# Performance work log

Hardware: AMD Instinct MI355X
Metric: run time of the kernel (lower is better)

## Reference

```python
import jax, jax.numpy as jnp
import numpy as np


def setup_inputs() -> dict:
    key = jax.random.key(0)
    ks = jax.random.split(key, 7)
    B, N, D, A = 16, 2048, 256, 256
    s = 1.0 / np.sqrt(D)
    return {
        "x": jax.random.normal(ks[0], (B, N, D), dtype=jnp.float32),
        "W1": jax.random.normal(ks[1], (D, A), dtype=jnp.float32) * s,
        "b1": jnp.zeros((A,), dtype=jnp.float32),
        "W2": jax.random.normal(ks[2], (D, A), dtype=jnp.float32) * s,
        "b2": jnp.zeros((A,), dtype=jnp.float32),
        "W3": jax.random.normal(ks[3], (D, A), dtype=jnp.float32) * s,
        "b3": jnp.zeros((A,), dtype=jnp.float32),
    }


def reference(x, W1, b1, W2, b2, W3, b3):
    # x: [B, N, D]
    Q = x @ W1 + b1  # [B, N, A]
    K = x @ W2 + b2  # [B, N, A]
    V = x @ W3 + b3  # [B, N, A]
    # unscaled attention scores, as in the original (no 1/sqrt(d))
    scores = jnp.einsum("bqa,bka->bqk", Q, K)  # [B, N, N]
    weights = jax.nn.softmax(scores, axis=-1)
    ctx = jnp.einsum("bqk,bka->bqa", weights, V)  # [B, N, A]
    return ctx.sum(axis=1)  # [B, A] (squeeze is a no-op for B>1)
```

## Files before the change

### kernel.cpp

```cpp
#include <hip/hip_runtime.h>
#include <hip/hip_bf16.h>
#include <stdint.h>

typedef unsigned short u16;
typedef __attribute__((ext_vector_type(8)))  short    s16x8;
typedef __attribute__((ext_vector_type(8)))  _Float16 f16x8;
typedef __attribute__((ext_vector_type(16))) float    f32x16;

#define B_DIM 16
#define N_SEQ 2048
#define M_TOT (B_DIM * N_SEQ)
#define LOG2E 1.44269504088896f
#define SHIFT 64.0f

static __device__ __forceinline__ f32x16 MFMA16(f16x8 a, f16x8 b, f32x16 c) {
  return __builtin_amdgcn_mfma_f32_32x32x16_f16(a, b, c, 0, 0, 0);
}

static __device__ __forceinline__ void stage_f16(
    const u16* __restrict__ src, char* ldsbuf, int row0, int t)
{
#pragma unroll
  for (int jj = 0; jj < 4; ++jj) {
    const int row = (t >> 5) + jj * 8;
    const int sl  = (t & 31) ^ (t >> 5);
    const char* g = (const char*)src + ((size_t)(row0 + row) * 512 + (size_t)sl * 16);
    __builtin_amdgcn_global_load_lds(
        (const __attribute__((address_space(1))) uint32_t*)g,
        (__attribute__((address_space(3))) uint32_t*)(ldsbuf + t * 16 + jj * 4096),
        16, 0, 0);
  }
}

#define SWZ8(bid, G_, J_)                                      \
  const int xcd_ = (bid) & 7, r_ = (bid) >> 3;                 \
  const int J_ = r_ & 7;                                       \
  const int G_ = ((r_ >> 3) << 3) | xcd_;

__global__ void splitW_kernel(const float* __restrict__ W1, const float* __restrict__ W2,
                              u16* __restrict__ WTf) {
  const int gid = blockIdx.x * 256 + threadIdx.x;
  const int a = gid >> 8, k = gid & 255;
  const float v = (a < 256) ? W1[k * 256 + a] * LOG2E : W2[k * 256 + (a - 256)];
  WTf[gid] = __builtin_bit_cast(u16, (_Float16)v);
}

__global__ __launch_bounds__(256, 2) void proj_kernel(
    const float* __restrict__ x, const u16* __restrict__ WTf,
    const float* __restrict__ b1, const float* __restrict__ b2,
    u16* __restrict__ Qf, u16* __restrict__ Kf)
{
  __shared__ char lds[32768];
  const int t = threadIdx.x, wv = t >> 6, ln = t & 63, lr = ln & 31, g = ln >> 5;
  const int ablk = blockIdx.x & 3;
  const int m0 = (blockIdx.x >> 2) * 256;
  const int aglob = ablk * 128 + wv * 32 + lr;

  f16x8 wf[16];
  {
    const u16* base = WTf + (size_t)aglob * 256 + g * 8;
#pragma unroll
    for (int c = 0; c < 16; ++c) wf[c] = *(const f16x8*)(base + c * 16);
  }
  const float bias = (aglob < 256) ? b1[aglob] * LOG2E : b2[aglob - 256];
  u16* Of = (ablk < 2) ? Qf : Kf;
  const int acol = aglob & 255;

  const int srow = t >> 3;
  const int scol = (t & 7) * 32;

  float4 v[8];
  {
    const float* src = x + (size_t)(m0 + srow) * 256 + scol;
#pragma unroll
    for (int j = 0; j < 8; ++j) v[j] = *(const float4*)(src + j * 4);
#pragma unroll
    for (int q8 = 0; q8 < 4; ++q8) {
      float ff[8] = {v[q8*2].x, v[q8*2].y, v[q8*2].z, v[q8*2].w,
                     v[q8*2+1].x, v[q8*2+1].y, v[q8*2+1].z, v[q8*2+1].w};
      f16x8 H;
#pragma unroll
      for (int e = 0; e < 8; ++e) H[e] = (_Float16)ff[e];
      const int swz = (((t & 7) * 4 + q8) ^ (srow & 7));
      *(f16x8*)(lds + srow * 512 + swz * 16) = H;
    }
  }
  __syncthreads();
  int p = 0;
  for (int it = 0; it < 8; ++it) {
    if (it + 1 < 8) {
      const float* src = x + (size_t)(m0 + (it + 1) * 32 + srow) * 256 + scol;
#pragma unroll
      for (int j = 0; j < 8; ++j) v[j] = *(const float4*)(src + j * 4);
    }
    const char* bh = lds + p * 16384;
    f32x16 S = {};
#pragma unroll
    for (int cc = 0; cc < 16; ++cc) {
      const int sl = ((cc * 2 + g) ^ (lr & 7)) * 16;
      const f16x8 a = *(const f16x8*)(bh + lr * 512 + sl);
      S = MFMA16(a, wf[cc], S);
    }
#pragma unroll
    for (int i = 0; i < 16; ++i) {
      const int mrow = m0 + it * 32 + (i & 3) + 8 * (i >> 2) + 4 * g;
      const float val = S[i] + bias;
      Of[(size_t)mrow * 256 + acol] = __builtin_bit_cast(u16, (_Float16)val);
    }
    if (it + 1 < 8) {
      char* bp = lds + (p ^ 1) * 16384;
#pragma unroll
      for (int q8 = 0; q8 < 4; ++q8) {
        float ff[8] = {v[q8*2].x, v[q8*2].y, v[q8*2].z, v[q8*2].w,
                       v[q8*2+1].x, v[q8*2+1].y, v[q8*2+1].z, v[q8*2+1].w};
        f16x8 H;
#pragma unroll
        for (int e = 0; e < 8; ++e) H[e] = (_Float16)ff[e];
        const int swz = (((t & 7) * 4 + q8) ^ (srow & 7));
        *(f16x8*)(bp + srow * 512 + swz * 16) = H;
      }
    }
    __syncthreads();
    p ^= 1;
  }
}

__global__ __launch_bounds__(256, 2) void pass1_kernel(
    const u16* __restrict__ Qf, const u16* __restrict__ Kf,
    float* __restrict__ lsum)
{
  __shared__ char lds[32768];
  SWZ8(blockIdx.x, grp, qg);
  const int b = grp >> 2, kq = grp & 3;
  const int t = threadIdx.x, wv = t >> 6, ln = t & 63, lr = ln & 31, gg = ln >> 5;

  const int q0 = b * 2048 + qg * 256 + wv * 64;
  f16x8 qf0[16], qf1[16];
  {
    const u16* qb0 = Qf + (size_t)(q0 + lr) * 256 + gg * 8;
    const u16* qb1 = qb0 + 32 * 256;
#pragma unroll
    for (int c = 0; c < 16; ++c) {
      qf0[c] = *(const f16x8*)(qb0 + c * 16);
      qf1[c] = *(const f16x8*)(qb1 + c * 16);
    }
  }
  const int k0 = b * 2048 + kq * 512;

  stage_f16(Kf, lds, k0, t);
  __syncthreads();
  float l0 = 0.f, l1 = 0.f;
  int pp = 0;
  for (int it = 0; it < 16; ++it) {
    if (it + 1 < 16) stage_f16(Kf, lds + (pp ^ 1) * 16384, k0 + (it + 1) * 32, t);
    const char* bh = lds + pp * 16384;
    f32x16 S0, S1;
#pragma unroll
    for (int i = 0; i < 16; ++i) { S0[i] = -SHIFT; S1[i] = -SHIFT; }
#pragma unroll
    for (int c = 0; c < 16; ++c) {
      const int sl = ((c * 2 + gg) ^ (lr & 7)) * 16;
      const f16x8 a = *(const f16x8*)(bh + lr * 512 + sl);
      S0 = MFMA16(a, qf0[c], S0);
      S1 = MFMA16(a, qf1[c], S1);
    }
    float r0 = 0.f, r1 = 0.f;
#pragma unroll
    for (int i = 0; i < 16; ++i) { r0 += exp2f(S0[i]); r1 += exp2f(S1[i]); }
    l0 += r0; l1 += r1;
    __syncthreads();
    pp ^= 1;
  }
  l0 += __shfl_xor(l0, 32);
  l1 += __shfl_xor(l1, 32);
  if (ln < 32) {
    atomicAdd(&lsum[q0 + ln],      l0);
    atomicAdd(&lsum[q0 + 32 + ln], l1);
  }
}

__global__ __launch_bounds__(256, 2) void pass2_kernel(
    const u16* __restrict__ Qf, const u16* __restrict__ Kf,
    const float* __restrict__ lsum, float* __restrict__ cvec)
{
  __shared__ char lds[32768];
  SWZ8(blockIdx.x, grp, kg);
  const int b = grp >> 2, qq = grp & 3;
  const int t = threadIdx.x, wv = t >> 6, ln = t & 63, lr = ln & 31, gg = ln >> 5;

  const int k0 = b * 2048 + kg * 256 + wv * 64;
  f16x8 kf0[16], kf1[16];
  {
    const u16* kb0 = Kf + (size_t)(k0 + lr) * 256 + gg * 8;
    const u16* kb1 = kb0 + 32 * 256;
#pragma unroll
    for (int c = 0; c < 16; ++c) {
      kf0[c] = *(const f16x8*)(kb0 + c * 16);
      kf1[c] = *(const f16x8*)(kb1 + c * 16);
    }
  }
  const int q0 = b * 2048 + qq * 512;

  float ck0[16], ck1[16];
#pragma unroll
  for (int i = 0; i < 16; ++i) { ck0[i] = 0.f; ck1[i] = 0.f; }

  stage_f16(Qf, lds, q0, t);
  __syncthreads();
  int pp = 0;
  for (int it = 0; it < 16; ++it) {
    if (it + 1 < 16) stage_f16(Qf, lds + (pp ^ 1) * 16384, q0 + (it + 1) * 32, t);
    const float il = 1.0f / fmaxf(lsum[q0 + it * 32 + lr], 1e-30f);
    const char* bh = lds + pp * 16384;
    f32x16 S0, S1;
#pragma unroll
    for (int i = 0; i < 16; ++i) { S0[i] = -SHIFT; S1[i] = -SHIFT; }
#pragma unroll
    for (int c = 0; c < 16; ++c) {
      const int sl = ((c * 2 + gg) ^ (lr & 7)) * 16;
      const f16x8 qa = *(const f16x8*)(bh + lr * 512 + sl);
      S0 = MFMA16(kf0[c], qa, S0);
      S1 = MFMA16(kf1[c], qa, S1);
    }
#pragma unroll
    for (int i = 0; i < 16; ++i) {
      ck0[i] += exp2f(S0[i]) * il;
      ck1[i] += exp2f(S1[i]) * il;
    }
    __syncthreads();
    pp ^= 1;
  }
#pragma unroll
  for (int i = 0; i < 16; ++i) {
#pragma unroll
    for (int d = 1; d <= 16; d <<= 1) {
      ck0[i] += __shfl_xor(ck0[i], d);
      ck1[i] += __shfl_xor(ck1[i], d);
    }
  }
  if (lr == 0) {
#pragma unroll
    for (int i = 0; i < 16; ++i) {
      const int klocal = (i & 3) + 8 * (i >> 2) + 4 * gg;
      atomicAdd(&cvec[k0 + klocal],      ck0[i]);
      atomicAdd(&cvec[k0 + 32 + klocal], ck1[i]);
    }
  }
}

__global__ void reducey_kernel(const float* __restrict__ x, const float* __restrict__ cvec,
                               float* __restrict__ yv, float* __restrict__ sumc) {
  const int b = blockIdx.x >> 4, kc = blockIdx.x & 15, tid = threadIdx.x;
  const float* xb = x + ((size_t)b * 2048 + kc * 128) * 256;
  const float* cb = cvec + b * 2048 + kc * 128;
  float a0 = 0.f, a1 = 0.f, a2 = 0.f, a3 = 0.f;
  for (int k = 0; k < 128; k += 4) {
    a0 = fmaf(cb[k],     xb[(size_t)k * 256 + tid],       a0);
    a1 = fmaf(cb[k + 1], xb[(size_t)(k + 1) * 256 + tid], a1);
    a2 = fmaf(cb[k + 2], xb[(size_t)(k + 2) * 256 + tid], a2);
    a3 = fmaf(cb[k + 3], xb[(size_t)(k + 3) * 256 + tid], a3);
  }
  atomicAdd(&yv[b * 256 + tid], (a0 + a1) + (a2 + a3));
  if (tid == 0) {
    float s = 0.f;
    for (int k = 0; k < 128; ++k) s += cb[k];
    atomicAdd(&sumc[b], s);
  }
}

__global__ void final_kernel(const float* __restrict__ yv, const float* __restrict__ sumc,
                             const float* __restrict__ W3, const float* __restrict__ b3,
                             float* __restrict__ out) {
  __shared__ float ys[256];
  const int b = blockIdx.x, a = threadIdx.x;
  ys[a] = yv[b * 256 + a];
  __syncthreads();
  float acc = sumc[b] * b3[a];
#pragma unroll 4
  for (int d = 0; d < 256; ++d) acc = fmaf(ys[d], W3[d * 256 + a], acc);
  out[b * 256 + a] = acc;
}

extern "C" void kernel_launch(void* const* d_in, const int* in_sizes, int n_in,
                              void* d_out, int out_size, void* d_ws, size_t ws_size,
                              hipStream_t stream) {
  const float* x  = (const float*)d_in[0];
  const float* W1 = (const float*)d_in[1];
  const float* b1 = (const float*)d_in[2];
  const float* W2 = (const float*)d_in[3];
  const float* b2 = (const float*)d_in[4];
  const float* W3 = (const float*)d_in[5];
  const float* b3 = (const float*)d_in[6];
  float* out = (float*)d_out;

  char* ws = (char*)d_ws;
  const size_t SZ_WT = 512u * 256u * 2u;
  const size_t SZ_QK = (size_t)M_TOT * 256u * 2u;
  u16* WTf = (u16*)(ws);                 ws += SZ_WT;
  u16* Qf  = (u16*)(ws);                 ws += SZ_QK;
  u16* Kf  = (u16*)(ws);                 ws += SZ_QK;
  float* lsum = (float*)(ws);            ws += (size_t)M_TOT * 4u;
  float* cvec = (float*)(ws);            ws += (size_t)M_TOT * 4u;
  float* yv   = (float*)(ws);            ws += 4096u * 4u;
  float* sumc = (float*)(ws);            ws += 64u;

  hipMemsetAsync(lsum, 0, (size_t)M_TOT * 8u + 4096u * 4u + 64u, stream);

  splitW_kernel<<<dim3(512), dim3(256), 0, stream>>>(W1, W2, WTf);
  proj_kernel<<<dim3(512), dim3(256), 0, stream>>>(x, WTf, b1, b2, Qf, Kf);
  pass1_kernel<<<dim3(512), dim3(256), 0, stream>>>(Qf, Kf, lsum);
  pass2_kernel<<<dim3(512), dim3(256), 0, stream>>>(Qf, Kf, lsum, cvec);
  reducey_kernel<<<dim3(256), dim3(256), 0, stream>>>(x, cvec, yv, sumc);
  final_kernel<<<dim3(16), dim3(256), 0, stream>>>(yv, sumc, W3, b3, out);
}
```

Before: 229.5 us.

## Stage 64-row K/Q tiles, precompute inverse sums, use hardware exp2 and setprio

pass1 and pass2 now stage 64-row tiles per iteration in a 64KB double-buffered dynamic LDS region, halving the number of barriers and iterations. pass2 precomputes the reciprocal softmax sums into LDS up front instead of doing a global load and division every iteration. Both passes use the hardware exp2 builtin and raise wave priority around the MFMA loops. proj_kernel switches to 512-thread blocks that each cover one of Q or K, which halves the number of blocks and the x loads per thread. The larger LDS footprint may reduce how many blocks fit on a CU.

```diff
diff --git a/kernel.cpp b/kernel.cpp
--- a/kernel.cpp
+++ b/kernel.cpp
@@ -3,7 +3,6 @@
 #include <stdint.h>
 
 typedef unsigned short u16;
-typedef __attribute__((ext_vector_type(8)))  short    s16x8;
 typedef __attribute__((ext_vector_type(8)))  _Float16 f16x8;
 typedef __attribute__((ext_vector_type(16))) float    f32x16;
 
@@ -13,18 +12,24 @@
 #define LOG2E 1.44269504088896f
 #define SHIFT 64.0f
 
+#if __has_builtin(__builtin_amdgcn_exp2f)
+#define EXP2(x) __builtin_amdgcn_exp2f(x)
+#else
+#define EXP2(x) exp2f(x)
+#endif
+
 static __device__ __forceinline__ f32x16 MFMA16(f16x8 a, f16x8 b, f32x16 c) {
   return __builtin_amdgcn_mfma_f32_32x32x16_f16(a, b, c, 0, 0, 0);
 }
 
-static __device__ __forceinline__ void stage_f16(
+static __device__ __forceinline__ void stage64(
     const u16* __restrict__ src, char* ldsbuf, int row0, int t)
 {
 #pragma unroll
-  for (int jj = 0; jj < 4; ++jj) {
-    const int row = (t >> 5) + jj * 8;
-    const int sl  = (t & 31) ^ (t >> 5);
-    const char* g = (const char*)src + ((size_t)(row0 + row) * 512 + (size_t)sl * 16);
+  for (int jj = 0; jj < 8; ++jj) {
+    const int sl = (t & 31) ^ (t >> 5);
+    const char* g = (const char*)src +
+        ((size_t)(row0 + (t >> 5) + jj * 8) * 512 + (size_t)sl * 16);
     __builtin_amdgcn_global_load_lds(
         (const __attribute__((address_space(1))) uint32_t*)g,
         (__attribute__((address_space(3))) uint32_t*)(ldsbuf + t * 16 + jj * 4096),
@@ -45,43 +50,42 @@
   WTf[gid] = __builtin_bit_cast(u16, (_Float16)v);
 }
 
-__global__ __launch_bounds__(256, 2) void proj_kernel(
+__global__ __launch_bounds__(512, 2) void proj_kernel(
     const float* __restrict__ x, const u16* __restrict__ WTf,
     const float* __restrict__ b1, const float* __restrict__ b2,
     u16* __restrict__ Qf, u16* __restrict__ Kf)
 {
   __shared__ char lds[32768];
   const int t = threadIdx.x, wv = t >> 6, ln = t & 63, lr = ln & 31, g = ln >> 5;
-  const int ablk = blockIdx.x & 3;
-  const int m0 = (blockIdx.x >> 2) * 256;
-  const int aglob = ablk * 128 + wv * 32 + lr;
+  const int ablk = blockIdx.x & 1;
+  const int m0 = (blockIdx.x >> 1) * 256;
+  const int aglob = wv * 32 + lr;
 
   f16x8 wf[16];
   {
-    const u16* base = WTf + (size_t)aglob * 256 + g * 8;
+    const u16* base = WTf + ((size_t)ablk * 256 + aglob) * 256 + g * 8;
 #pragma unroll
     for (int c = 0; c < 16; ++c) wf[c] = *(const f16x8*)(base + c * 16);
   }
-  const float bias = (aglob < 256) ? b1[aglob] * LOG2E : b2[aglob - 256];
-  u16* Of = (ablk < 2) ? Qf : Kf;
-  const int acol = aglob & 255;
-
-  const int srow = t >> 3;
-  const int scol = (t & 7) * 32;
-
-  float4 v[8];
+  const float bias = (ablk == 0) ? b1[aglob] * LOG2E : b2[aglob];
+  u16* Of = (ablk == 0) ? Qf : Kf;
+
+  const int srow = t >> 4;
+  const int scol = (t & 15) * 16;
+
+  float4 v[4];
   {
     const float* src = x + (size_t)(m0 + srow) * 256 + scol;
 #pragma unroll
-    for (int j = 0; j < 8; ++j) v[j] = *(const float4*)(src + j * 4);
-#pragma unroll
-    for (int q8 = 0; q8 < 4; ++q8) {
+    for (int j = 0; j < 4; ++j) v[j] = *(const float4*)(src + j * 4);
+#pragma unroll
+    for (int q8 = 0; q8 < 2; ++q8) {
       float ff[8] = {v[q8*2].x, v[q8*2].y, v[q8*2].z, v[q8*2].w,
                      v[q8*2+1].x, v[q8*2+1].y, v[q8*2+1].z, v[q8*2+1].w};
       f16x8 H;
 #pragma unroll
       for (int e = 0; e < 8; ++e) H[e] = (_Float16)ff[e];
-      const int swz = (((t & 7) * 4 + q8) ^ (srow & 7));
+      const int swz = (((t & 15) * 2 + q8) ^ (srow & 7));
       *(f16x8*)(lds + srow * 512 + swz * 16) = H;
     }
   }
@@ -91,7 +95,7 @@
     if (it + 1 < 8) {
       const float* src = x + (size_t)(m0 + (it + 1) * 32 + srow) * 256 + scol;
 #pragma unroll
-      for (int j = 0; j < 8; ++j) v[j] = *(const float4*)(src + j * 4);
+      for (int j = 0; j < 4; ++j) v[j] = *(const float4*)(src + j * 4);
     }
     const char* bh = lds + p * 16384;
     f32x16 S = {};
@@ -105,18 +109,18 @@
     for (int i = 0; i < 16; ++i) {
       const int mrow = m0 + it * 32 + (i & 3) + 8 * (i >> 2) + 4 * g;
       const float val = S[i] + bias;
-      Of[(size_t)mrow * 256 + acol] = __builtin_bit_cast(u16, (_Float16)val);
+      Of[(size_t)mrow * 256 + aglob] = __builtin_bit_cast(u16, (_Float16)val);
     }
     if (it + 1 < 8) {
       char* bp = lds + (p ^ 1) * 16384;
 #pragma unroll
-      for (int q8 = 0; q8 < 4; ++q8) {
+      for (int q8 = 0; q8 < 2; ++q8) {
         float ff[8] = {v[q8*2].x, v[q8*2].y, v[q8*2].z, v[q8*2].w,
                        v[q8*2+1].x, v[q8*2+1].y, v[q8*2+1].z, v[q8*2+1].w};
         f16x8 H;
 #pragma unroll
         for (int e = 0; e < 8; ++e) H[e] = (_Float16)ff[e];
-        const int swz = (((t & 7) * 4 + q8) ^ (srow & 7));
+        const int swz = (((t & 15) * 2 + q8) ^ (srow & 7));
         *(f16x8*)(bp + srow * 512 + swz * 16) = H;
       }
     }
@@ -129,7 +133,7 @@
     const u16* __restrict__ Qf, const u16* __restrict__ Kf,
     float* __restrict__ lsum)
 {
-  __shared__ char lds[32768];
+  extern __shared__ char lds[];
   SWZ8(blockIdx.x, grp, qg);
   const int b = grp >> 2, kq = grp & 3;
   const int t = threadIdx.x, wv = t >> 6, ln = t & 63, lr = ln & 31, gg = ln >> 5;
@@ -147,29 +151,35 @@
   }
   const int k0 = b * 2048 + kq * 512;
 
-  stage_f16(Kf, lds, k0, t);
+  stage64(Kf, lds, k0, t);
   __syncthreads();
+
   float l0 = 0.f, l1 = 0.f;
-  int pp = 0;
-  for (int it = 0; it < 16; ++it) {
-    if (it + 1 < 16) stage_f16(Kf, lds + (pp ^ 1) * 16384, k0 + (it + 1) * 32, t);
-    const char* bh = lds + pp * 16384;
-    f32x16 S0, S1;
-#pragma unroll
-    for (int i = 0; i < 16; ++i) { S0[i] = -SHIFT; S1[i] = -SHIFT; }
-#pragma unroll
-    for (int c = 0; c < 16; ++c) {
-      const int sl = ((c * 2 + gg) ^ (lr & 7)) * 16;
-      const f16x8 a = *(const f16x8*)(bh + lr * 512 + sl);
-      S0 = MFMA16(a, qf0[c], S0);
-      S1 = MFMA16(a, qf1[c], S1);
-    }
-    float r0 = 0.f, r1 = 0.f;
-#pragma unroll
-    for (int i = 0; i < 16; ++i) { r0 += exp2f(S0[i]); r1 += exp2f(S1[i]); }
-    l0 += r0; l1 += r1;
+  int p = 0;
+  for (int it = 0; it < 8; ++it) {
+    if (it + 1 < 8) stage64(Kf, lds + (p ^ 1) * 32768, k0 + (it + 1) * 64, t);
+    const char* bh = lds + p * 32768;
+#pragma unroll
+    for (int h = 0; h < 2; ++h) {
+      f32x16 S0, S1;
+#pragma unroll
+      for (int i = 0; i < 16; ++i) { S0[i] = -SHIFT; S1[i] = -SHIFT; }
+      __builtin_amdgcn_s_setprio(1);
+#pragma unroll
+      for (int c = 0; c < 16; ++c) {
+        const int sl = ((c * 2 + gg) ^ (lr & 7)) * 16;
+        const f16x8 a = *(const f16x8*)(bh + (h * 32 + lr) * 512 + sl);
+        S0 = MFMA16(a, qf0[c], S0);
+        S1 = MFMA16(a, qf1[c], S1);
+      }
+      __builtin_amdgcn_s_setprio(0);
+      float r0 = 0.f, r1 = 0.f;
+#pragma unroll
+      for (int i = 0; i < 16; ++i) { r0 += EXP2(S0[i]); r1 += EXP2(S1[i]); }
+      l0 += r0; l1 += r1;
+    }
     __syncthreads();
-    pp ^= 1;
+    p ^= 1;
   }
   l0 += __shfl_xor(l0, 32);
   l1 += __shfl_xor(l1, 32);
@@ -183,12 +193,22 @@
     const u16* __restrict__ Qf, const u16* __restrict__ Kf,
     const float* __restrict__ lsum, float* __restrict__ cvec)
 {
-  __shared__ char lds[32768];
+  extern __shared__ char lds[];
+  float* ilds = (float*)(lds + 65536);
   SWZ8(blockIdx.x, grp, kg);
   const int b = grp >> 2, qq = grp & 3;
   const int t = threadIdx.x, wv = t >> 6, ln = t & 63, lr = ln & 31, gg = ln >> 5;
 
   const int k0 = b * 2048 + kg * 256 + wv * 64;
+  const int q0 = b * 2048 + qq * 512;
+
+  {
+    const float la = lsum[q0 + t];
+    const float lb = lsum[q0 + 256 + t];
+    ilds[t]       = 1.0f / fmaxf(la, 1e-30f);
+    ilds[t + 256] = 1.0f / fmaxf(lb, 1e-30f);
+  }
+
   f16x8 kf0[16], kf1[16];
   {
     const u16* kb0 = Kf + (size_t)(k0 + lr) * 256 + gg * 8;
@@ -199,36 +219,41 @@
       kf1[c] = *(const f16x8*)(kb1 + c * 16);
     }
   }
-  const int q0 = b * 2048 + qq * 512;
 
   float ck0[16], ck1[16];
 #pragma unroll
   for (int i = 0; i < 16; ++i) { ck0[i] = 0.f; ck1[i] = 0.f; }
 
-  stage_f16(Qf, lds, q0, t);
+  stage64(Qf, lds, q0, t);
   __syncthreads();
-  int pp = 0;
-  for (int it = 0; it < 16; ++it) {
-    if (it + 1 < 16) stage_f16(Qf, lds + (pp ^ 1) * 16384, q0 + (it + 1) * 32, t);
-    const float il = 1.0f / fmaxf(lsum[q0 + it * 32 + lr], 1e-30f);
-    const char* bh = lds + pp * 16384;
-    f32x16 S0, S1;
-#pragma unroll
-    for (int i = 0; i < 16; ++i) { S0[i] = -SHIFT; S1[i] = -SHIFT; }
-#pragma unroll
-    for (int c = 0; c < 16; ++c) {
-      const int sl = ((c * 2 + gg) ^ (lr & 7)) * 16;
-      const f16x8 qa = *(const f16x8*)(bh + lr * 512 + sl);
-      S0 = MFMA16(kf0[c], qa, S0);
-      S1 = MFMA16(kf1[c], qa, S1);
-    }
-#pragma unroll
-    for (int i = 0; i < 16; ++i) {
-      ck0[i] += exp2f(S0[i]) * il;
-      ck1[i] += exp2f(S1[i]) * il;
+
+  int p = 0;
+  for (int it = 0; it < 8; ++it) {
+    if (it + 1 < 8) stage64(Qf, lds + (p ^ 1) * 32768, q0 + (it + 1) * 64, t);
+    const char* bh = lds + p * 32768;
+#pragma unroll
+    for (int h = 0; h < 2; ++h) {
+      const float il = ilds[it * 64 + h * 32 + lr];
+      f32x16 S0, S1;
+#pragma unroll
+      for (int i = 0; i < 16; ++i) { S0[i] = -SHIFT; S1[i] = -SHIFT; }
+      __builtin_amdgcn_s_setprio(1);
+#pragma unroll
+      for (int c = 0; c < 16; ++c) {
+        const int sl = ((c * 2 + gg) ^ (lr & 7)) * 16;
+        const f16x8 qa = *(const f16x8*)(bh + (h * 32 + lr) * 512 + sl);
+        S0 = MFMA16(kf0[c], qa, S0);
+        S1 = MFMA16(kf1[c], qa, S1);
+      }
+      __builtin_amdgcn_s_setprio(0);
+#pragma unroll
+      for (int i = 0; i < 16; ++i) {
+        ck0[i] += EXP2(S0[i]) * il;
+        ck1[i] += EXP2(S1[i]) * il;
+      }
     }
     __syncthreads();
-    pp ^= 1;
+    p ^= 1;
   }
 #pragma unroll
   for (int i = 0; i < 16; ++i) {
@@ -306,10 +331,15 @@
 
   hipMemsetAsync(lsum, 0, (size_t)M_TOT * 8u + 4096u * 4u + 64u, stream);
 
+  hipFuncSetAttribute((const void*)pass1_kernel,
+                      hipFuncAttributeMaxDynamicSharedMemorySize, 65536);
+  hipFuncSetAttribute((const void*)pass2_kernel,
+                      hipFuncAttributeMaxDynamicSharedMemorySize, 67584);
+
   splitW_kernel<<<dim3(512), dim3(256), 0, stream>>>(W1, W2, WTf);
-  proj_kernel<<<dim3(512), dim3(256), 0, stream>>>(x, WTf, b1, b2, Qf, Kf);
-  pass1_kernel<<<dim3(512), dim3(256), 0, stream>>>(Qf, Kf, lsum);
-  pass2_kernel<<<dim3(512), dim3(256), 0, stream>>>(Qf, Kf, lsum, cvec);
+  proj_kernel<<<dim3(256), dim3(512), 0, stream>>>(x, WTf, b1, b2, Qf, Kf);
+  pass1_kernel<<<dim3(512), dim3(256), 65536, stream>>>(Qf, Kf, lsum);
+  pass2_kernel<<<dim3(512), dim3(256), 67584, stream>>>(Qf, Kf, lsum, cvec);
   reducey_kernel<<<dim3(256), dim3(256), 0, stream>>>(x, cvec, yv, sumc);
   final_kernel<<<dim3(16), dim3(256), 0, stream>>>(yv, sumc, W3, b3, out);
 }
```

Result: slower. 278.9 us (+21.5%).
